# Kernel optimization log

Measured on AMD Instinct MI355X. Metric: run time of the kernel, lower is better.

The kernel has to match this reference:

```python
import jax, jax.numpy as jnp
import numpy as np

N = 8192
D = 256
ALPHA = 0.2  # LeakyReLU negative slope
NEG_INF = -9e15


def setup_inputs() -> dict:
    key = jax.random.key(0)
    k1, k2, k3, k4, k5, k6 = jax.random.split(key, 6)
    inputs = jax.random.normal(k1, (N, D), dtype=jnp.float32)
    # sparse random binary adjacency, avg degree ~32, plus self loops
    adj = (jax.random.uniform(k2, (N, N)) < (32.0 / N)).astype(jnp.float32)
    adj = jnp.maximum(adj, jnp.eye(N, dtype=jnp.float32))
    cmt_weight = jax.random.uniform(k3, (N, 1), dtype=jnp.float32)  # unused by SPGAT
    W = jax.random.normal(k4, (D, D), dtype=jnp.float32) * (1.0 / np.sqrt(D))
    a1 = jax.random.normal(k5, (D, 1), dtype=jnp.float32) * 0.1
    a2 = jax.random.normal(k6, (D, 1), dtype=jnp.float32) * 0.1
    return {"inputs": inputs, "adj": adj, "cmt_weight": cmt_weight,
            "W": W, "a1": a1, "a2": a2}


def reference(inputs, adj, cmt_weight, W, a1, a2):
    # SPGAT (batched GAT layer with batch=1, squeezed):
    Wh = inputs @ W                       # [N, D]
    f1 = Wh @ a1                          # [N, 1]
    f2 = Wh @ a2                          # [N, 1]
    e = jax.nn.leaky_relu(f1 + f2.T, negative_slope=ALPHA)  # [N, N]
    scores = jnp.where(adj > 0, e, NEG_INF)
    att = jax.nn.softmax(scores, axis=-1)  # [N, N]
    node_out = jax.nn.relu(att @ Wh)       # [N, D]
    return node_out
```

## Files before the change

### kernel.cpp

```cpp
#include <hip/hip_runtime.h>
#include <hip/hip_bf16.h>
#include <math.h>

#define NN 8192
#define DD 256
#define DEG_CAP 128
#define GEMM_NB (NN / 32)
#define SCAN_NB (NN / 4)
constexpr float ALPHA = 0.2f;

typedef __attribute__((ext_vector_type(4))) float f32x4;
typedef __attribute__((ext_vector_type(8))) short bf16x8;
typedef __attribute__((ext_vector_type(8))) unsigned short u16x8;

__global__ __launch_bounds__(256) void k_convW(const float* __restrict__ W,
                                               short* __restrict__ WhiT,
                                               short* __restrict__ WloT) {
    __shared__ float tile[64][65];
    const int n0 = (blockIdx.x & 3) * 64;
    const int k0 = (blockIdx.x >> 2) * 64;
    const int c = threadIdx.x & 63;
    const int rg = threadIdx.x >> 6;
    #pragma unroll
    for (int i = 0; i < 16; ++i) {
        int r = rg * 16 + i;
        tile[r][c] = W[(size_t)(k0 + r) * DD + n0 + c];
    }
    __syncthreads();
    #pragma unroll
    for (int i = 0; i < 16; ++i) {
        int rw = rg * 16 + i;
        float x = tile[c][rw];
        __hip_bfloat16 hb = __float2bfloat16(x);
        float hf = __bfloat162float(hb);
        __hip_bfloat16 lb = __float2bfloat16(x - hf);
        WhiT[(size_t)(n0 + rw) * DD + k0 + c] = __builtin_bit_cast(short, hb);
        WloT[(size_t)(n0 + rw) * DD + k0 + c] = __builtin_bit_cast(short, lb);
    }
}

#define LDAx 32
__global__ __launch_bounds__(256) void k_fused(const float* __restrict__ X,
                                               const float* __restrict__ adj,
                                               const short* __restrict__ WhiT,
                                               const short* __restrict__ WloT,
                                               const float* __restrict__ a1,
                                               const float* __restrict__ a2,
                                               unsigned short* __restrict__ Whb,
                                               float* __restrict__ f1,
                                               float* __restrict__ f2,
                                               int* __restrict__ cnt,
                                               int* __restrict__ ej) {
    __shared__ short sAh[32 * LDAx], sAl[32 * LDAx];
    __shared__ short sBh[256 * LDAx], sBl[256 * LDAx];
    __shared__ float sP[2][2][32];
    const int tid = threadIdx.x;
    const int lane = tid & 63;
    const int wid = tid >> 6;
    if (blockIdx.x < GEMM_NB) {
        const int wm = wid >> 1, wn = wid & 1;
        const int row0 = blockIdx.x * 32;
        f32x4 acc[4][2] = {};
        for (int k0 = 0; k0 < DD; k0 += 32) {
            {
                int r = tid >> 3, c4 = tid & 7;
                f32x4 xv = *(const f32x4*)(X + (size_t)(row0 + r) * DD + k0 + c4 * 4);
                short hx[4], lx[4];
                #pragma unroll
                for (int q = 0; q < 4; ++q) {
                    __hip_bfloat16 hb = __float2bfloat16(xv[q]);
                    float hf = __bfloat162float(hb);
                    __hip_bfloat16 lb = __float2bfloat16(xv[q] - hf);
                    hx[q] = __builtin_bit_cast(short, hb);
                    lx[q] = __builtin_bit_cast(short, lb);
                }
                *(short4*)(sAh + r * LDAx + c4 * 4) = make_short4(hx[0], hx[1], hx[2], hx[3]);
                *(short4*)(sAl + r * LDAx + c4 * 4) = make_short4(lx[0], lx[1], lx[2], lx[3]);
                const int4* srcH = (const int4*)(WhiT + (size_t)tid * DD + k0);
                const int4* srcL = (const int4*)(WloT + (size_t)tid * DD + k0);
                #pragma unroll
                for (int j = 0; j < 4; ++j) {
                    *(int4*)(sBh + tid * LDAx + j * 8) = srcH[j];
                    *(int4*)(sBl + tid * LDAx + j * 8) = srcL[j];
                }
            }
            __syncthreads();
            const int kb = (lane >> 4) * 8;
            const int l15 = lane & 15;
            bf16x8 ah = *(const bf16x8*)(sAh + (wm * 16 + l15) * LDAx + kb);
            bf16x8 al = *(const bf16x8*)(sAl + (wm * 16 + l15) * LDAx + kb);
            #pragma unroll
            for (int ct = 0; ct < 4; ++ct)
                #pragma unroll
                for (int ni = 0; ni < 2; ++ni) {
                    int br = ct * 64 + wn * 32 + ni * 16 + l15;
                    bf16x8 bh = *(const bf16x8*)(sBh + br * LDAx + kb);
                    bf16x8 bl = *(const bf16x8*)(sBl + br * LDAx + kb);
                    acc[ct][ni] = __builtin_amdgcn_mfma_f32_16x16x32_bf16(ah, bh, acc[ct][ni], 0, 0, 0);
                    acc[ct][ni] = __builtin_amdgcn_mfma_f32_16x16x32_bf16(ah, bl, acc[ct][ni], 0, 0, 0);
                    acc[ct][ni] = __builtin_amdgcn_mfma_f32_16x16x32_bf16(al, bh, acc[ct][ni], 0, 0, 0);
                }
            __syncthreads();
        }
        const int l15 = lane & 15;
        const int orow = row0 + wm * 16 + (lane >> 4) * 4;
        float s1[4] = {0.f, 0.f, 0.f, 0.f}, s2[4] = {0.f, 0.f, 0.f, 0.f};
        #pragma unroll
        for (int ct = 0; ct < 4; ++ct)
            #pragma unroll
            for (int ni = 0; ni < 2; ++ni) {
                int cc = ct * 64 + wn * 32 + ni * 16 + l15;
                float A1 = a1[cc], A2 = a2[cc];
                #pragma unroll
                for (int r = 0; r < 4; ++r) {
                    float x = acc[ct][ni][r];
                    Whb[(size_t)(orow + r) * DD + cc] =
                        __builtin_bit_cast(unsigned short, __float2bfloat16(x));
                    s1[r] = fmaf(x, A1, s1[r]);
                    s2[r] = fmaf(x, A2, s2[r]);
                }
            }
        #pragma unroll
        for (int o = 1; o < 16; o <<= 1)
            #pragma unroll
            for (int r = 0; r < 4; ++r) {
                s1[r] += __shfl_xor(s1[r], o);
                s2[r] += __shfl_xor(s2[r], o);
            }
        if (l15 == 0) {
            #pragma unroll
            for (int r = 0; r < 4; ++r) {
                int lr = wm * 16 + (lane >> 4) * 4 + r;
                sP[0][wn][lr] = s1[r];
                sP[1][wn][lr] = s2[r];
            }
        }
        __syncthreads();
        if (tid < 32) {
            f1[row0 + tid] = sP[0][0][tid] + sP[0][1][tid];
            f2[row0 + tid] = sP[1][0][tid] + sP[1][1][tid];
        }
    } else {
        const int row = (blockIdx.x - GEMM_NB) * 4 + wid;
        const f32x4* arow = (const f32x4*)(adj + (size_t)row * NN);
        int* erow = ej + (size_t)row * DEG_CAP;
        int base = 0;
        for (int sc = 0; sc < 2; ++sc) {
            f32x4 v[16];
            #pragma unroll
            for (int u = 0; u < 16; ++u)
                v[u] = __builtin_nontemporal_load(&arow[sc * 1024 + u * 64 + lane]);
            #pragma unroll
            for (int u = 0; u < 16; ++u) {
                #pragma unroll
                for (int q = 0; q < 4; ++q) {
                    bool hit = v[u][q] > 0.f;
                    unsigned long long mask = __ballot(hit);
                    if (hit) {
                        int pos = base + __popcll(mask & ((1ull << lane) - 1ull));
                        if (pos < DEG_CAP)
                            erow[pos] = (sc * 1024 + u * 64 + lane) * 4 + q;
                    }
                    base += __popcll(mask);
                }
            }
        }
        if (lane == 0) cnt[row] = base < DEG_CAP ? base : DEG_CAP;
    }
}

__global__ __launch_bounds__(256) void k_agg(const int* __restrict__ cnt,
                                             const int* __restrict__ ej,
                                             const unsigned short* __restrict__ Whb,
                                             const float* __restrict__ f1,
                                             const float* __restrict__ f2,
                                             float* __restrict__ out) {
    __shared__ int   s_j[4][DEG_CAP];
    __shared__ float s_e[4][DEG_CAP];
    const int tid = threadIdx.x;
    const int lane = tid & 63, wid = tid >> 6;
    const int row = blockIdx.x * 4 + wid;
    int cw = cnt[row];
    cw = cw < DEG_CAP ? cw : DEG_CAP;
    const float f1i = f1[row];
    const int* erow = ej + (size_t)row * DEG_CAP;
    float e0 = -INFINITY, e1 = -INFINITY;
    if (lane < cw) {
        int j = erow[lane];
        s_j[wid][lane] = j;
        float e = f1i + f2[j];
        e0 = e > 0.f ? e : ALPHA * e;
        s_e[wid][lane] = e0;
    }
    if (lane + 64 < cw) {
        int j = erow[lane + 64];
        s_j[wid][lane + 64] = j;
        float e = f1i + f2[j];
        e1 = e > 0.f ? e : ALPHA * e;
        s_e[wid][lane + 64] = e1;
    }
    float mx = fmaxf(e0, e1);
    #pragma unroll
    for (int o = 32; o; o >>= 1) mx = fmaxf(mx, __shfl_xor(mx, o));
    float sm = __expf(e0 - mx) + __expf(e1 - mx);
    #pragma unroll
    for (int o = 32; o; o >>= 1) sm += __shfl_xor(sm, o);
    const int half = lane >> 5, sl = lane & 31;
    const int* sj = s_j[wid];
    const float* se = s_e[wid];
    f32x4 accA = {0.f, 0.f, 0.f, 0.f};
    f32x4 accB = {0.f, 0.f, 0.f, 0.f};
    {
        auto ld = [&](int kk) -> u16x8 {
            int idx = kk + half;
            int j = sj[idx < cw ? idx : 0];
            return *(const u16x8*)(Whb + (size_t)j * DD + sl * 8);
        };
        u16x8 b0 = ld(0), b1 = ld(2), b2 = ld(4), b3 = ld(6);
        for (int kk = 0; kk < cw; kk += 8) {
            #pragma unroll
            for (int p = 0; p < 4; ++p) {
                u16x8 cur = p == 0 ? b0 : p == 1 ? b1 : p == 2 ? b2 : b3;
                int idx = kk + p * 2 + half;
                float w = idx < cw ? __expf(se[idx] - mx) : 0.f;
                #pragma unroll
                for (int q = 0; q < 4; ++q) {
                    float lo = __builtin_bit_cast(float, (unsigned)cur[2 * q] << 16);
                    float hi = __builtin_bit_cast(float, (unsigned)cur[2 * q + 1] << 16);
                    if (q < 2) {
                        accA[2 * q]     = fmaf(w, lo, accA[2 * q]);
                        accA[2 * q + 1] = fmaf(w, hi, accA[2 * q + 1]);
                    } else {
                        accB[2 * (q - 2)]     = fmaf(w, lo, accB[2 * (q - 2)]);
                        accB[2 * (q - 2) + 1] = fmaf(w, hi, accB[2 * (q - 2) + 1]);
                    }
                }
            }
            b0 = ld(kk + 8); b1 = ld(kk + 10); b2 = ld(kk + 12); b3 = ld(kk + 14);
        }
    }
    #pragma unroll
    for (int q = 0; q < 4; ++q) {
        accA[q] += __shfl_xor(accA[q], 32);
        accB[q] += __shfl_xor(accB[q], 32);
    }
    const float inv = 1.f / sm;
    if (half == 0) {
        f32x4 r0, r1;
        #pragma unroll
        for (int q = 0; q < 4; ++q) {
            float oa = accA[q] * inv, ob = accB[q] * inv;
            r0[q] = oa > 0.f ? oa : 0.f;
            r1[q] = ob > 0.f ? ob : 0.f;
        }
        float* op = out + (size_t)row * DD + sl * 8;
        __builtin_nontemporal_store(r0, (f32x4*)op);
        __builtin_nontemporal_store(r1, (f32x4*)(op + 4));
    }
}

extern "C" void kernel_launch(void* const* d_in, const int* in_sizes, int n_in,
                              void* d_out, int out_size, void* d_ws, size_t ws_size,
                              hipStream_t stream) {
    const float* X   = (const float*)d_in[0];
    const float* adj = (const float*)d_in[1];
    const float* W   = (const float*)d_in[3];
    const float* a1  = (const float*)d_in[4];
    const float* a2  = (const float*)d_in[5];
    float* out = (float*)d_out;

    short* WhiT = (short*)d_ws;
    short* WloT = WhiT + (size_t)DD * DD;
    float* f1   = (float*)(WloT + (size_t)DD * DD);
    float* f2   = f1 + NN;
    unsigned short* Whb = (unsigned short*)(f2 + NN);
    int*   cnt  = (int*)(Whb + (size_t)NN * DD);
    int*   ej   = cnt + NN;

    k_convW<<<16, 256, 0, stream>>>(W, WhiT, WloT);
    k_fused<<<GEMM_NB + SCAN_NB, 256, 0, stream>>>(X, adj, WhiT, WloT, a1, a2,
                                                   Whb, f1, f2, cnt, ej);
    k_agg<<<NN / 4, 256, 0, stream>>>(cnt, ej, Whb, f1, f2, out);
}
```

Baseline: 78.07 us.

## Split adjacency scan across kernels to overlap with aggregation

Splits the adjacency scan into two halves. The first half runs alongside the GEMM. The second half runs in the same launch as aggregation of the first half of rows, and a third kernel aggregates the remaining rows. The intent is to overlap the bandwidth-heavy adjacency scan with the gather-bound aggregation and balance work across launches. This adds an extra kernel launch and a dependency boundary.

New measurement: 87.45 us. 12.0% more time.

```diff
diff --git a/kernel.cpp b/kernel.cpp
--- a/kernel.cpp
+++ b/kernel.cpp
@@ -6,7 +6,7 @@
 #define DD 256
 #define DEG_CAP 128
 #define GEMM_NB (NN / 32)
-#define SCAN_NB (NN / 4)
+#define HALF_NB (NN / 8)
 constexpr float ALPHA = 0.2f;
 
 typedef __attribute__((ext_vector_type(4))) float f32x4;
@@ -39,18 +39,133 @@
     }
 }
 
+__device__ __forceinline__ void scan_row(int row, int lane,
+                                         const float* __restrict__ adj,
+                                         int* __restrict__ cnt,
+                                         int* __restrict__ ej) {
+    const f32x4* arow = (const f32x4*)(adj + (size_t)row * NN);
+    int* erow = ej + (size_t)row * DEG_CAP;
+    int base = 0;
+    for (int sc = 0; sc < 2; ++sc) {
+        f32x4 v[16];
+        #pragma unroll
+        for (int u = 0; u < 16; ++u)
+            v[u] = __builtin_nontemporal_load(&arow[sc * 1024 + u * 64 + lane]);
+        #pragma unroll
+        for (int u = 0; u < 16; ++u) {
+            #pragma unroll
+            for (int q = 0; q < 4; ++q) {
+                bool hit = v[u][q] > 0.f;
+                unsigned long long mask = __ballot(hit);
+                if (hit) {
+                    int pos = base + __popcll(mask & ((1ull << lane) - 1ull));
+                    if (pos < DEG_CAP)
+                        erow[pos] = (sc * 1024 + u * 64 + lane) * 4 + q;
+                }
+                base += __popcll(mask);
+            }
+        }
+    }
+    if (lane == 0) cnt[row] = base < DEG_CAP ? base : DEG_CAP;
+}
+
+__device__ __forceinline__ void agg_row(int row, int lane,
+                                        int* __restrict__ sj, float* __restrict__ se,
+                                        const int* __restrict__ cnt,
+                                        const int* __restrict__ ej,
+                                        const unsigned short* __restrict__ Whb,
+                                        const float* __restrict__ f1,
+                                        const float* __restrict__ f2,
+                                        float* __restrict__ out) {
+    int cw = cnt[row];
+    cw = cw < DEG_CAP ? cw : DEG_CAP;
+    const float f1i = f1[row];
+    const int* erow = ej + (size_t)row * DEG_CAP;
+    float e0 = -INFINITY, e1 = -INFINITY;
+    if (lane < cw) {
+        int j = erow[lane];
+        sj[lane] = j;
+        float e = f1i + f2[j];
+        e0 = e > 0.f ? e : ALPHA * e;
+        se[lane] = e0;
+    }
+    if (lane + 64 < cw) {
+        int j = erow[lane + 64];
+        sj[lane + 64] = j;
+        float e = f1i + f2[j];
+        e1 = e > 0.f ? e : ALPHA * e;
+        se[lane + 64] = e1;
+    }
+    float mx = fmaxf(e0, e1);
+    #pragma unroll
+    for (int o = 32; o; o >>= 1) mx = fmaxf(mx, __shfl_xor(mx, o));
+    float sm = __expf(e0 - mx) + __expf(e1 - mx);
+    #pragma unroll
+    for (int o = 32; o; o >>= 1) sm += __shfl_xor(sm, o);
+    const int half = lane >> 5, sl = lane & 31;
+    f32x4 accA = {0.f, 0.f, 0.f, 0.f};
+    f32x4 accB = {0.f, 0.f, 0.f, 0.f};
+    {
+        auto ld = [&](int kk) -> u16x8 {
+            int idx = kk + half;
+            int j = sj[idx < cw ? idx : 0];
+            return *(const u16x8*)(Whb + (size_t)j * DD + sl * 8);
+        };
+        u16x8 b0 = ld(0), b1 = ld(2), b2 = ld(4), b3 = ld(6);
+        for (int kk = 0; kk < cw; kk += 8) {
+            #pragma unroll
+            for (int p = 0; p < 4; ++p) {
+                u16x8 cur = p == 0 ? b0 : p == 1 ? b1 : p == 2 ? b2 : b3;
+                int idx = kk + p * 2 + half;
+                float w = idx < cw ? __expf(se[idx] - mx) : 0.f;
+                #pragma unroll
+                for (int q = 0; q < 4; ++q) {
+                    float lo = __builtin_bit_cast(float, (unsigned)cur[2 * q] << 16);
+                    float hi = __builtin_bit_cast(float, (unsigned)cur[2 * q + 1] << 16);
+                    if (q < 2) {
+                        accA[2 * q]     = fmaf(w, lo, accA[2 * q]);
+                        accA[2 * q + 1] = fmaf(w, hi, accA[2 * q + 1]);
+                    } else {
+                        accB[2 * (q - 2)]     = fmaf(w, lo, accB[2 * (q - 2)]);
+                        accB[2 * (q - 2) + 1] = fmaf(w, hi, accB[2 * (q - 2) + 1]);
+                    }
+                }
+            }
+            b0 = ld(kk + 8); b1 = ld(kk + 10); b2 = ld(kk + 12); b3 = ld(kk + 14);
+        }
+    }
+    #pragma unroll
+    for (int q = 0; q < 4; ++q) {
+        accA[q] += __shfl_xor(accA[q], 32);
+        accB[q] += __shfl_xor(accB[q], 32);
+    }
+    const float inv = 1.f / sm;
+    if (half == 0) {
+        f32x4 r0, r1;
+        #pragma unroll
+        for (int q = 0; q < 4; ++q) {
+            float oa = accA[q] * inv, ob = accB[q] * inv;
+            r0[q] = oa > 0.f ? oa : 0.f;
+            r1[q] = ob > 0.f ? ob : 0.f;
+        }
+        float* op = out + (size_t)row * DD + sl * 8;
+        __builtin_nontemporal_store(r0, (f32x4*)op);
+        __builtin_nontemporal_store(r1, (f32x4*)(op + 4));
+    }
+}
+
 #define LDAx 32
-__global__ __launch_bounds__(256) void k_fused(const float* __restrict__ X,
-                                               const float* __restrict__ adj,
-                                               const short* __restrict__ WhiT,
-                                               const short* __restrict__ WloT,
-                                               const float* __restrict__ a1,
-                                               const float* __restrict__ a2,
-                                               unsigned short* __restrict__ Whb,
-                                               float* __restrict__ f1,
-                                               float* __restrict__ f2,
-                                               int* __restrict__ cnt,
-                                               int* __restrict__ ej) {
+__global__ __launch_bounds__(256) void k_gemmscan(const float* __restrict__ X,
+                                                  const float* __restrict__ adj,
+                                                  const short* __restrict__ WhiT,
+                                                  const short* __restrict__ WloT,
+                                                  const float* __restrict__ a1,
+                                                  const float* __restrict__ a2,
+                                                  unsigned short* __restrict__ Whb,
+                                                  float* __restrict__ f1,
+                                                  float* __restrict__ f2,
+                                                  int* __restrict__ cnt,
+                                                  int* __restrict__ ej) {
     __shared__ short sAh[32 * LDAx], sAl[32 * LDAx];
     __shared__ short sBh[256 * LDAx], sBl[256 * LDAx];
     __shared__ float sP[2][2][32];
@@ -142,121 +257,40 @@
         }
     } else {
         const int row = (blockIdx.x - GEMM_NB) * 4 + wid;
-        const f32x4* arow = (const f32x4*)(adj + (size_t)row * NN);
-        int* erow = ej + (size_t)row * DEG_CAP;
-        int base = 0;
-        for (int sc = 0; sc < 2; ++sc) {
-            f32x4 v[16];
-            #pragma unroll
-            for (int u = 0; u < 16; ++u)
-                v[u] = __builtin_nontemporal_load(&arow[sc * 1024 + u * 64 + lane]);
-            #pragma unroll
-            for (int u = 0; u < 16; ++u) {
-                #pragma unroll
-                for (int q = 0; q < 4; ++q) {
-                    bool hit = v[u][q] > 0.f;
-                    unsigned long long mask = __ballot(hit);
-                    if (hit) {
-                        int pos = base + __popcll(mask & ((1ull << lane) - 1ull));
-                        if (pos < DEG_CAP)
-                            erow[pos] = (sc * 1024 + u * 64 + lane) * 4 + q;
-                    }
-                    base += __popcll(mask);
-                }
-            }
-        }
-        if (lane == 0) cnt[row] = base < DEG_CAP ? base : DEG_CAP;
-    }
-}
-
-__global__ __launch_bounds__(256) void k_agg(const int* __restrict__ cnt,
-                                             const int* __restrict__ ej,
-                                             const unsigned short* __restrict__ Whb,
-                                             const float* __restrict__ f1,
-                                             const float* __restrict__ f2,
-                                             float* __restrict__ out) {
+        scan_row(row, lane, adj, cnt, ej);
+    }
+}
+
+__global__ __launch_bounds__(256) void k_scanagg(const float* __restrict__ adj,
+                                                 const unsigned short* __restrict__ Whb,
+                                                 const float* __restrict__ f1,
+                                                 const float* __restrict__ f2,
+                                                 int* __restrict__ cnt,
+                                                 int* __restrict__ ej,
+                                                 float* __restrict__ out) {
     __shared__ int   s_j[4][DEG_CAP];
     __shared__ float s_e[4][DEG_CAP];
-    const int tid = threadIdx.x;
-    const int lane = tid & 63, wid = tid >> 6;
-    const int row = blockIdx.x * 4 + wid;
-    int cw = cnt[row];
-    cw = cw < DEG_CAP ? cw : DEG_CAP;
-    const float f1i = f1[row];
-    const int* erow = ej + (size_t)row * DEG_CAP;
-    float e0 = -INFINITY, e1 = -INFINITY;
-    if (lane < cw) {
-        int j = erow[lane];
-        s_j[wid][lane] = j;
-        float e = f1i + f2[j];
-        e0 = e > 0.f ? e : ALPHA * e;
-        s_e[wid][lane] = e0;
-    }
-    if (lane + 64 < cw) {
-        int j = erow[lane + 64];
-        s_j[wid][lane + 64] = j;
-        float e = f1i + f2[j];
-        e1 = e > 0.f ? e : ALPHA * e;
-        s_e[wid][lane + 64] = e1;
-    }
-    float mx = fmaxf(e0, e1);
-    #pragma unroll
-    for (int o = 32; o; o >>= 1) mx = fmaxf(mx, __shfl_xor(mx, o));
-    float sm = __expf(e0 - mx) + __expf(e1 - mx);
-    #pragma unroll
-    for (int o = 32; o; o >>= 1) sm += __shfl_xor(sm, o);
-    const int half = lane >> 5, sl = lane & 31;
-    const int* sj = s_j[wid];
-    const float* se = s_e[wid];
-    f32x4 accA = {0.f, 0.f, 0.f, 0.f};
-    f32x4 accB = {0.f, 0.f, 0.f, 0.f};
-    {
-        auto ld = [&](int kk) -> u16x8 {
-            int idx = kk + half;
-            int j = sj[idx < cw ? idx : 0];
-            return *(const u16x8*)(Whb + (size_t)j * DD + sl * 8);
-        };
-        u16x8 b0 = ld(0), b1 = ld(2), b2 = ld(4), b3 = ld(6);
-        for (int kk = 0; kk < cw; kk += 8) {
-            #pragma unroll
-            for (int p = 0; p < 4; ++p) {
-                u16x8 cur = p == 0 ? b0 : p == 1 ? b1 : p == 2 ? b2 : b3;
-                int idx = kk + p * 2 + half;
-                float w = idx < cw ? __expf(se[idx] - mx) : 0.f;
-                #pragma unroll
-                for (int q = 0; q < 4; ++q) {
-                    float lo = __builtin_bit_cast(float, (unsigned)cur[2 * q] << 16);
-                    float hi = __builtin_bit_cast(float, (unsigned)cur[2 * q + 1] << 16);
-                    if (q < 2) {
-                        accA[2 * q]     = fmaf(w, lo, accA[2 * q]);
-                        accA[2 * q + 1] = fmaf(w, hi, accA[2 * q + 1]);
-                    } else {
-                        accB[2 * (q - 2)]     = fmaf(w, lo, accB[2 * (q - 2)]);
-                        accB[2 * (q - 2) + 1] = fmaf(w, hi, accB[2 * (q - 2) + 1]);
-                    }
-                }
-            }
-            b0 = ld(kk + 8); b1 = ld(kk + 10); b2 = ld(kk + 12); b3 = ld(kk + 14);
-        }
-    }
-    #pragma unroll
-    for (int q = 0; q < 4; ++q) {
-        accA[q] += __shfl_xor(accA[q], 32);
-        accB[q] += __shfl_xor(accB[q], 32);
-    }
-    const float inv = 1.f / sm;
-    if (half == 0) {
-        f32x4 r0, r1;
-        #pragma unroll
-        for (int q = 0; q < 4; ++q) {
-            float oa = accA[q] * inv, ob = accB[q] * inv;
-            r0[q] = oa > 0.f ? oa : 0.f;
-            r1[q] = ob > 0.f ? ob : 0.f;
-        }
-        float* op = out + (size_t)row * DD + sl * 8;
-        __builtin_nontemporal_store(r0, (f32x4*)op);
-        __builtin_nontemporal_store(r1, (f32x4*)(op + 4));
-    }
+    const int lane = threadIdx.x & 63, wid = threadIdx.x >> 6;
+    if (blockIdx.x < HALF_NB) {
+        const int row = NN / 2 + blockIdx.x * 4 + wid;
+        scan_row(row, lane, adj, cnt, ej);
+    } else {
+        const int row = (blockIdx.x - HALF_NB) * 4 + wid;
+        agg_row(row, lane, s_j[wid], s_e[wid], cnt, ej, Whb, f1, f2, out);
+    }
+}
+
+__global__ __launch_bounds__(256) void k_agg2(const int* __restrict__ cnt,
+                                              const int* __restrict__ ej,
+                                              const unsigned short* __restrict__ Whb,
+                                              const float* __restrict__ f1,
+                                              const float* __restrict__ f2,
+                                              float* __restrict__ out) {
+    __shared__ int   s_j[4][DEG_CAP];
+    __shared__ float s_e[4][DEG_CAP];
+    const int lane = threadIdx.x & 63, wid = threadIdx.x >> 6;
+    const int row = NN / 2 + blockIdx.x * 4 + wid;
+    agg_row(row, lane, s_j[wid], s_e[wid], cnt, ej, Whb, f1, f2, out);
 }
 
 extern "C" void kernel_launch(void* const* d_in, const int* in_sizes, int n_in,
@@ -278,7 +312,8 @@
     int*   ej   = cnt + NN;
 
     k_convW<<<16, 256, 0, stream>>>(W, WhiT, WloT);
-    k_fused<<<GEMM_NB + SCAN_NB, 256, 0, stream>>>(X, adj, WhiT, WloT, a1, a2,
-                                                   Whb, f1, f2, cnt, ej);
-    k_agg<<<NN / 4, 256, 0, stream>>>(cnt, ej, Whb, f1, f2, out);
-}
+    k_gemmscan<<<GEMM_NB + HALF_NB, 256, 0, stream>>>(X, adj, WhiT, WloT, a1, a2,
+                                                      Whb, f1, f2, cnt, ej);
+    k_scanagg<<<2 * HALF_NB, 256, 0, stream>>>(adj, Whb, f1, f2, cnt, ej, out);
+    k_agg2<<<HALF_NB, 256, 0, stream>>>(cnt, ej, Whb, f1, f2, out);
+}
```
